# Performance work log

Measured on AMD Instinct MI355X. Metric: run time of the kernel, lower is better.

Reference implementation:

```python
import jax, jax.numpy as jnp
import numpy as np
import math

N, E, D, H = 1536, 49152, 512, 8
DH = D // H  # head dim = 64
SCALE = 256.0 * math.sqrt(2.0)  # rel_dists scaling in forward


def sinusoidal_pe(x, d):
    """x: [...] float positions -> [..., d] interleaved sin/cos encoding."""
    div = jnp.exp(jnp.arange(0, d, 2, dtype=jnp.float32) * (-math.log(10000.0) / d))
    ang = x[..., None] * div  # [..., d//2]
    return jnp.stack([jnp.sin(ang), jnp.cos(ang)], axis=-1).reshape(*x.shape, d)


def setup_inputs() -> dict:
    key = jax.random.key(0)
    ks = jax.random.split(key, 8)
    features = jax.random.normal(ks[0], (N, D), dtype=jnp.float32)
    edge_index = jax.random.randint(ks[1], (2, E), 0, N, dtype=jnp.int64)
    edge_attr = jax.random.uniform(ks[2], (E,), dtype=jnp.float32)  # normalized distances
    pos = jax.random.uniform(ks[3], (N, 2), dtype=jnp.float32)  # unused by forward
    s = 1.0 / math.sqrt(D)  # ~xavier-uniform bound sqrt(6/(D+D))... use simple symmetric init
    Wq = jax.random.uniform(ks[4], (D, D), minval=-s, maxval=s, dtype=jnp.float32)
    Wk = jax.random.uniform(ks[5], (D, D), minval=-s, maxval=s, dtype=jnp.float32)
    Wv = jax.random.uniform(ks[6], (D, D), minval=-s, maxval=s, dtype=jnp.float32)
    bq = jnp.zeros((D,), jnp.float32)
    bk = jnp.zeros((D,), jnp.float32)
    bv = jnp.zeros((D,), jnp.float32)
    return dict(features=features, edge_index=edge_index, edge_attr=edge_attr, pos=pos,
                Wq=Wq, bq=bq, Wk=Wk, bk=bk, Wv=Wv, bv=bv)


def reference(features, edge_index, edge_attr, pos, Wq, bq, Wk, bk, Wv, bv):
    # batch dim is 1 in the original (features.unsqueeze(0)); we omit it.
    q = (features @ Wq.T + bq).reshape(N, H, DH).transpose(1, 0, 2)  # [H,N,DH]
    k = (features @ Wk.T + bk).reshape(N, H, DH).transpose(1, 0, 2)
    v = (features @ Wv.T + bv).reshape(N, H, DH).transpose(1, 0, 2)

    qk = jnp.einsum('hqd,hrd->hqr', q, k)  # [H,N,N]

    # to_dense_adj: scatter-add edge_attr into dense [N,N], then scale
    rel = jnp.zeros((N, N), jnp.float32).at[edge_index[0], edge_index[1]].add(edge_attr) * SCALE
    # embed_k and embed_q are identical parameter-free sinusoidal encodings of rel
    rk = sinusoidal_pe(rel, DH)  # [N,N,DH]

    # original: qk + q.rk + k.rq + (q_repeat*k_repeat == qk)  => 2*qk + q.rk + k.rk
    logits = 2.0 * qk \
        + jnp.einsum('hqd,qrd->hqr', q, rk) \
        + jnp.einsum('hrd,qrd->hqr', k, rk)
    attn = jax.nn.softmax(logits / math.sqrt(DH), axis=-1)  # [H,N,N]

    out = jnp.einsum('hqr,hrd->hqd', attn, v)  # [H,N,DH]
    out = out.transpose(1, 0, 2).reshape(N, D)  # [N,D]
    return out.max(axis=0)  # [D] max-pool over nodes (MIL pooling)
```

## Files before the change

kernel.cpp:

```cpp
#include <hip/hip_runtime.h>
#include <cmath>


constexpr int Nn  = 1536;
constexpr int Dd  = 512;
constexpr int Hh  = 8;
constexpr int DHd = 64;
constexpr int SPLITS = 4;
constexpr float SCALE_F = 362.03867196751236f;
constexpr float M0 = 8.0f;

typedef float f4 __attribute__((ext_vector_type(4)));
typedef int   i4 __attribute__((ext_vector_type(4)));
typedef unsigned short us4 __attribute__((ext_vector_type(4)));
typedef __attribute__((ext_vector_type(4))) float f32x4;
typedef __attribute__((ext_vector_type(8))) short bf16x8;

__device__ inline unsigned short bf16_rne(float x) {
    unsigned u = __float_as_uint(x);
    unsigned r = u + 0x7fff + ((u >> 16) & 1);
    return (unsigned short)(r >> 16);
}
__device__ inline float bf16_tof(unsigned short h) {
    return __uint_as_float(((unsigned)h) << 16);
}
__device__ inline unsigned f2ord(float x) {
    unsigned b = __float_as_uint(x);
    return (b & 0x80000000u) ? ~b : (b | 0x80000000u);
}

__global__ __launch_bounds__(256) void setup_k(
    const float* __restrict__ feat,
    const float* __restrict__ Wq, const float* __restrict__ Wk, const float* __restrict__ Wv,
    unsigned short* __restrict__ pFh, unsigned short* __restrict__ pFl,
    unsigned short* __restrict__ pWh, unsigned short* __restrict__ pWl,
    float* __restrict__ rel, unsigned short* __restrict__ eid16,
    float* __restrict__ Obuf, float* __restrict__ Lbuf,
    float* __restrict__ qkodd, unsigned* __restrict__ ordmax)
{
    const int b = blockIdx.x, tid = threadIdx.x;
    if (b < 768) {
        int type = (b >= 384);
        int tg = (type ? (b - 384) : b) * 256 + tid;
        int L = tg & 63;
        int kc = (tg >> 6) & 15;
        int t10 = tg >> 10;
        const float* src;
        unsigned short *oh, *ol;
        int row, col;
        if (type == 0) {
            src = feat; oh = pFh; ol = pFl;
            row = t10 * 16 + (L & 15);
            col = kc * 32 + (L >> 4) * 8;
        } else {
            int z = t10 >> 5, nt = t10 & 31;
            src = (z == 0) ? Wq : (z == 1) ? Wk : Wv;
            oh = pWh; ol = pWl;
            row = nt * 16 + (L & 15);
            col = kc * 32 + (L >> 4) * 8;
        }
        f4 a = *(const f4*)(src + (size_t)row * Dd + col);
        f4 bb = *(const f4*)(src + (size_t)row * Dd + col + 4);
        float x[8];
        #pragma unroll
        for (int j = 0; j < 4; ++j) { x[j] = a[j]; x[4 + j] = bb[j]; }
        unsigned short hs[8], ls[8];
        #pragma unroll
        for (int j = 0; j < 8; ++j) {
            hs[j] = bf16_rne(x[j]);
            ls[j] = bf16_rne(x[j] - bf16_tof(hs[j]));
        }
        *(bf16x8*)(oh + (size_t)tg * 8) = *(bf16x8*)hs;
        *(bf16x8*)(ol + (size_t)tg * 8) = *(bf16x8*)ls;
    } else if (b < 3072) {
        size_t idx = (size_t)(b - 768) * 256 + tid;
        *(f4*)(rel + idx * 4) = (f4){0.f, 0.f, 0.f, 0.f};
        *(us4*)(eid16 + idx * 4) = (us4){0xFFFFu, 0xFFFFu, 0xFFFFu, 0xFFFFu};
    } else if (b < 3840) {
        size_t idx = (size_t)(b - 3072) * 256 + tid;
        *(f4*)(Obuf + idx * 4) = (f4){0.f, 0.f, 0.f, 0.f};
    } else if (b < 3852) {
        size_t idx = (size_t)(b - 3840) * 256 + tid;
        *(f4*)(Lbuf + idx * 4) = (f4){0.f, 0.f, 0.f, 0.f};
    } else if (b < 3876) {
        size_t idx = (size_t)(b - 3852) * 256 + tid;
        *(f4*)(qkodd + idx * 4) = (f4){0.f, 0.f, 0.f, 0.f};
    } else {
        int idx = (b - 3876) * 256 + tid;
        ordmax[idx] = 0x007FFFFFu;
    }
}

__global__ __launch_bounds__(256) void qkvm_k(
    const unsigned short* __restrict__ pFh, const unsigned short* __restrict__ pFl,
    const unsigned short* __restrict__ pWh, const unsigned short* __restrict__ pWl,
    const float* __restrict__ bq, const float* __restrict__ bk, const float* __restrict__ bv,
    float* __restrict__ Qo, float* __restrict__ Ko,
    float* __restrict__ qodd, float* __restrict__ kodd,
    unsigned short* __restrict__ pQh, unsigned short* __restrict__ pQl,
    unsigned short* __restrict__ pKh, unsigned short* __restrict__ pKl,
    unsigned short* __restrict__ pVh, unsigned short* __restrict__ pVl)
{
    const int z = blockIdx.z;
    const float* __restrict__ bias = (z == 0) ? bq : (z == 1) ? bk : bv;
    const int tid = threadIdx.x;
    const int L = tid & 63, wv = tid >> 6;
    const int l15 = L & 15, quad = L >> 4;
    const int mt0 = blockIdx.y * 4 + (wv & 1) * 2;
    const int nt0 = blockIdx.x * 4 + (wv >> 1) * 2;
    __shared__ float lds[4][32][33];

    f32x4 acc[2][2];
    #pragma unroll
    for (int i = 0; i < 2; ++i)
        #pragma unroll
        for (int j = 0; j < 2; ++j) acc[i][j] = (f32x4){0.f, 0.f, 0.f, 0.f};

    bf16x8 AH[2][2], AL[2][2], BH[2][2], BL[2][2];
    auto loadset = [&](int buf, int kc) {
        #pragma unroll
        for (int i = 0; i < 2; ++i) {
            size_t ao = ((size_t)((mt0 + i) * 16 + kc)) * 512 + L * 8;
            AH[buf][i] = *(const bf16x8*)(pFh + ao);
            AL[buf][i] = *(const bf16x8*)(pFl + ao);
            size_t bo = ((size_t)((z * 32 + nt0 + i) * 16 + kc)) * 512 + L * 8;
            BH[buf][i] = *(const bf16x8*)(pWh + bo);
            BL[buf][i] = *(const bf16x8*)(pWl + bo);
        }
    };
    auto mfmaset = [&](int buf) {
        #pragma unroll
        for (int i = 0; i < 2; ++i)
            #pragma unroll
            for (int j = 0; j < 2; ++j) {
                f32x4 a = acc[i][j];
                a = __builtin_amdgcn_mfma_f32_16x16x32_bf16(AH[buf][i], BH[buf][j], a, 0, 0, 0);
                a = __builtin_amdgcn_mfma_f32_16x16x32_bf16(AH[buf][i], BL[buf][j], a, 0, 0, 0);
                a = __builtin_amdgcn_mfma_f32_16x16x32_bf16(AL[buf][i], BH[buf][j], a, 0, 0, 0);
                a = __builtin_amdgcn_mfma_f32_16x16x32_bf16(AL[buf][i], BL[buf][j], a, 0, 0, 0);
                acc[i][j] = a;
            }
    };

    loadset(0, 0);
    #pragma unroll
    for (int kc = 0; kc < 16; kc += 2) {
        loadset(1, kc + 1);
        mfmaset(0);
        if (kc + 2 < 16) loadset(0, kc + 2);
        mfmaset(1);
    }

    float o_[2][2][4];
    #pragma unroll
    for (int i = 0; i < 2; ++i)
        #pragma unroll
        for (int j = 0; j < 2; ++j) {
            float b = bias[(nt0 + j) * 16 + l15];
            #pragma unroll
            for (int reg = 0; reg < 4; ++reg) o_[i][j][reg] = acc[i][j][reg] + b;
        }
    if (z < 2) {
        float* __restrict__ outp = (z == 0) ? Qo : Ko;
        #pragma unroll
        for (int i = 0; i < 2; ++i) {
            int row0 = (mt0 + i) * 16 + quad * 4;
            #pragma unroll
            for (int j = 0; j < 2; ++j) {
                int col = (nt0 + j) * 16 + l15;
                #pragma unroll
                for (int reg = 0; reg < 4; ++reg)
                    outp[(size_t)(row0 + reg) * Dd + col] = o_[i][j][reg];
            }
        }
        float* __restrict__ odst = (z == 0) ? qodd : kodd;
        const int h = blockIdx.x;
        #pragma unroll
        for (int i = 0; i < 2; ++i) {
            #pragma unroll
            for (int reg = 0; reg < 4; ++reg) {
                float v = (l15 & 1) ? (o_[i][0][reg] + o_[i][1][reg]) : 0.f;
                #pragma unroll
                for (int o = 1; o < 16; o <<= 1) v += __shfl_xor(v, o);
                if (l15 == 0) {
                    int row = (mt0 + i) * 16 + quad * 4 + reg;
                    atomicAdd(&odst[row * Hh + h], v);
                }
            }
        }
    }
    #pragma unroll
    for (int i = 0; i < 2; ++i)
        #pragma unroll
        for (int j = 0; j < 2; ++j)
            #pragma unroll
            for (int reg = 0; reg < 4; ++reg)
                lds[wv][i * 16 + quad * 4 + reg][j * 16 + l15] = o_[i][j][reg];

    const int h = blockIdx.x;
    if (z < 2) {
        unsigned short* __restrict__ oh = z ? pKh : pQh;
        unsigned short* __restrict__ ol = z ? pKl : pQl;
        const int kc = wv >> 1;
        const float sc = z ? 1.0f : 0.25f;
        #pragma unroll
        for (int i = 0; i < 2; ++i) {
            float x[8]; unsigned short hs[8], ls[8];
            #pragma unroll
            for (int j2 = 0; j2 < 8; ++j2)
                x[j2] = lds[wv][i * 16 + l15][quad * 8 + j2] * sc;
            #pragma unroll
            for (int j2 = 0; j2 < 8; ++j2) {
                hs[j2] = bf16_rne(x[j2]);
                ls[j2] = bf16_rne(x[j2] - bf16_tof(hs[j2]));
            }
            size_t off = ((size_t)((h * 96 + mt0 + i) * 2 + kc)) * 512 + L * 8;
            *(bf16x8*)(oh + off) = *(bf16x8*)hs;
            *(bf16x8*)(ol + off) = *(bf16x8*)ls;
        }
    } else {
        const int rc = blockIdx.y * 2 + (wv & 1);
        #pragma unroll
        for (int dtl = 0; dtl < 2; ++dtl) {
            int dt = (wv >> 1) * 2 + dtl;
            float x[8]; unsigned short hs[8], ls[8];
            #pragma unroll
            for (int j2 = 0; j2 < 8; ++j2)
                x[j2] = lds[wv][quad * 8 + j2][dtl * 16 + l15];
            #pragma unroll
            for (int j2 = 0; j2 < 8; ++j2) {
                hs[j2] = bf16_rne(x[j2]);
                ls[j2] = bf16_rne(x[j2] - bf16_tof(hs[j2]));
            }
            size_t off = ((size_t)((h * 48 + rc) * 4 + dt)) * 512 + L * 8;
            *(bf16x8*)(pVh + off) = *(bf16x8*)hs;
            *(bf16x8*)(pVl + off) = *(bf16x8*)ls;
        }
    }
}

__global__ __launch_bounds__(256) void scatter_k(
    const int* __restrict__ raw, const float* __restrict__ attr,
    float* __restrict__ rel, unsigned short* __restrict__ eid16,
    int* __restrict__ idxn, int E)
{
    int e = blockIdx.x * 256 + threadIdx.x;
    if (e >= E) return;
    int acc = 0;
    #pragma unroll
    for (int i = 0; i < 16; ++i) acc |= raw[2 * i + 1];
    int s, t;
    if (acc == 0) { s = raw[2 * e]; t = raw[2 * (E + e)]; }
    else          { s = raw[e];     t = raw[E + e]; }
    idxn[e] = s; idxn[E + e] = t;
    size_t off = (size_t)s * Nn + t;
    atomicAdd(rel + off, attr[e] * SCALE_F);
    eid16[off] = (unsigned short)e;
}

__global__ __launch_bounds__(256) void delta_k(
    const int* __restrict__ idxn, const float* __restrict__ rel,
    const float* __restrict__ Q, const float* __restrict__ K,
    const float* __restrict__ qodd, const float* __restrict__ kodd,
    float* __restrict__ delta8, int E)
{
    int t = blockIdx.x * 256 + threadIdx.x;
    if (t >= E * Hh) return;
    int e = t >> 3, h = t & 7;
    int qi = idxn[e], ri = idxn[E + e];
    float x = rel[(size_t)qi * Nn + ri];
    const float* qrow = Q + (size_t)qi * Dd + h * DHd;
    const float* krow = K + (size_t)ri * Dd + h * DHd;
    float acc = 0.f;
    #pragma unroll
    for (int i = 0; i < 32; i += 2) {
        float dd0 = 0.15915494309189535f * __builtin_amdgcn_exp2f(-0.4152410118609203f * (float)i);
        float dd1 = 0.15915494309189535f * __builtin_amdgcn_exp2f(-0.4152410118609203f * (float)(i + 1));
        float r0 = x * dd0; r0 -= floorf(r0);
        float r1 = x * dd1; r1 -= floorf(r1);
        float s0 = __builtin_amdgcn_sinf(r0), c0 = __builtin_amdgcn_cosf(r0);
        float s1 = __builtin_amdgcn_sinf(r1), c1 = __builtin_amdgcn_cosf(r1);
        f4 q4 = *(const f4*)(qrow + 2 * i);
        f4 k4 = *(const f4*)(krow + 2 * i);
        acc += (q4[0] + k4[0]) * s0 + (q4[1] + k4[1]) * c0
             + (q4[2] + k4[2]) * s1 + (q4[3] + k4[3]) * c1;
    }
    delta8[(size_t)e * Hh + h] = 0.125f * (acc - qodd[qi * Hh + h] - kodd[ri * Hh + h]);
}

__global__ __launch_bounds__(64, 3) void flash7_k(
    const unsigned short* __restrict__ pQh, const unsigned short* __restrict__ pQl,
    const unsigned short* __restrict__ pKh, const unsigned short* __restrict__ pKl,
    const unsigned short* __restrict__ pVh, const unsigned short* __restrict__ pVl,
    const unsigned short* __restrict__ eid16, const float* __restrict__ delta8,
    const float* __restrict__ kodd,
    float* __restrict__ Obuf, float* __restrict__ Lbuf)
{
    const int qt = blockIdx.x, h = blockIdx.y, s = blockIdx.z;
    const int L = threadIdx.x, quad = L >> 4, l15 = L & 15;
    const int q0 = qt * 16;
    __shared__ unsigned short phi[16][80];
    __shared__ unsigned short plo[16][80];

    bf16x8 qh[2], ql[2];
    #pragma unroll
    for (int kc = 0; kc < 2; ++kc) {
        size_t off = ((size_t)((h * 96 + qt) * 2 + kc)) * 512 + L * 8;
        qh[kc] = *(const bf16x8*)(pQh + off);
        ql[kc] = *(const bf16x8*)(pQl + off);
    }

    f32x4 O[4];
    float lsum[4];
    #pragma unroll
    for (int r = 0; r < 4; ++r) { lsum[r] = 0.f; O[r] = (f32x4){0.f, 0.f, 0.f, 0.f}; }

    const int NT = 24 / SPLITS;
    const int Tbase = s * NT;

    bf16x8 kh0[4], kh1[4], kl0[4], kl1[4];
    {
        const int r0 = Tbase * 64;
        #pragma unroll
        for (int nt = 0; nt < 4; ++nt) {
            size_t b0 = ((size_t)((h * 96 + (r0 >> 4) + nt) * 2)) * 512 + L * 8;
            kh0[nt] = *(const bf16x8*)(pKh + b0);
            kh1[nt] = *(const bf16x8*)(pKh + b0 + 512);
            kl0[nt] = *(const bf16x8*)(pKl + b0);
            kl1[nt] = *(const bf16x8*)(pKl + b0 + 512);
        }
    }

    float kvcur[4], dcur[16];
    {
        const int r0 = Tbase * 64;
        int ecur[16];
        #pragma unroll
        for (int nt = 0; nt < 4; ++nt) {
            kvcur[nt] = 0.125f * kodd[(size_t)(r0 + nt * 16 + l15) * Hh + h];
            #pragma unroll
            for (int reg = 0; reg < 4; ++reg) {
                unsigned short uv = eid16[(size_t)(q0 + quad * 4 + reg) * Nn + r0 + nt * 16 + l15];
                ecur[nt * 4 + reg] = (uv == 0xFFFFu) ? -1 : (int)uv;
            }
        }
        #pragma unroll
        for (int i = 0; i < 16; ++i) {
            int e = ecur[i];
            float d = delta8[(size_t)(e < 0 ? 0 : e) * Hh + h];
            dcur[i] = (e >= 0) ? d : 0.f;
        }
    }

    for (int T = 0; T < NT; ++T) {
        const int r0 = (Tbase + T) * 64;
        const bool more = (T + 1 < NT);

        int   enxt[16];
        float kvnxt[4];
        if (more) {
            const int r1 = r0 + 64;
            #pragma unroll
            for (int nt = 0; nt < 4; ++nt) {
                kvnxt[nt] = 0.125f * kodd[(size_t)(r1 + nt * 16 + l15) * Hh + h];
                #pragma unroll
                for (int reg = 0; reg < 4; ++reg) {
                    unsigned short uv = eid16[(size_t)(q0 + quad * 4 + reg) * Nn + r1 + nt * 16 + l15];
                    enxt[nt * 4 + reg] = (uv == 0xFFFFu) ? -1 : (int)uv;
                }
            }
        }

        bf16x8 vh0[4], vh1[4], vl0[4], vl1[4];
        #pragma unroll
        for (int dt = 0; dt < 4; ++dt) {
            size_t vb = ((size_t)((h * 48 + (r0 >> 5)) * 4 + dt)) * 512 + L * 8;
            vh0[dt] = *(const bf16x8*)(pVh + vb);
            vh1[dt] = *(const bf16x8*)(pVh + vb + 2048);
            vl0[dt] = *(const bf16x8*)(pVl + vb);
            vl1[dt] = *(const bf16x8*)(pVl + vb + 2048);
        }

        f32x4 S[4];
        #pragma unroll
        for (int nt = 0; nt < 4; ++nt) {
            f32x4 a = {0.f, 0.f, 0.f, 0.f};
            a = __builtin_amdgcn_mfma_f32_16x16x32_bf16(qh[0], kh0[nt], a, 0, 0, 0);
            a = __builtin_amdgcn_mfma_f32_16x16x32_bf16(qh[1], kh1[nt], a, 0, 0, 0);
            a = __builtin_amdgcn_mfma_f32_16x16x32_bf16(qh[0], kl0[nt], a, 0, 0, 0);
            a = __builtin_amdgcn_mfma_f32_16x16x32_bf16(qh[1], kl1[nt], a, 0, 0, 0);
            a = __builtin_amdgcn_mfma_f32_16x16x32_bf16(ql[0], kh0[nt], a, 0, 0, 0);
            a = __builtin_amdgcn_mfma_f32_16x16x32_bf16(ql[1], kh1[nt], a, 0, 0, 0);
            S[nt] = a;
        }

        if (more) {
            const int r1 = r0 + 64;
            #pragma unroll
            for (int nt = 0; nt < 4; ++nt) {
                size_t b0 = ((size_t)((h * 96 + (r1 >> 4) + nt) * 2)) * 512 + L * 8;
                kh0[nt] = *(const bf16x8*)(pKh + b0);
                kh1[nt] = *(const bf16x8*)(pKh + b0 + 512);
                kl0[nt] = *(const bf16x8*)(pKl + b0);
                kl1[nt] = *(const bf16x8*)(pKl + b0 + 512);
            }
        }

        #pragma unroll
        for (int reg = 0; reg < 4; ++reg) {
            float p[4];
            #pragma unroll
            for (int nt = 0; nt < 4; ++nt) {
                p[nt] = __expf(S[nt][reg] + kvcur[nt] + dcur[nt * 4 + reg] - M0);
                lsum[reg] += p[nt];
                unsigned short hi = bf16_rne(p[nt]);
                phi[quad * 4 + reg][nt * 16 + l15] = hi;
                plo[quad * 4 + reg][nt * 16 + l15] = bf16_rne(p[nt] - bf16_tof(hi));
            }
        }

        bf16x8 ph[2], pl[2];
        #pragma unroll
        for (int kc2 = 0; kc2 < 2; ++kc2) {
            ph[kc2] = *(const bf16x8*)&phi[l15][kc2 * 32 + quad * 8];
            pl[kc2] = *(const bf16x8*)&plo[l15][kc2 * 32 + quad * 8];
        }

        #pragma unroll
        for (int dt = 0; dt < 4; ++dt) {
            f32x4 a = O[dt];
            a = __builtin_amdgcn_mfma_f32_16x16x32_bf16(ph[0], vh0[dt], a, 0, 0, 0);
            a = __builtin_amdgcn_mfma_f32_16x16x32_bf16(ph[1], vh1[dt], a, 0, 0, 0);
            a = __builtin_amdgcn_mfma_f32_16x16x32_bf16(ph[0], vl0[dt], a, 0, 0, 0);
            a = __builtin_amdgcn_mfma_f32_16x16x32_bf16(ph[1], vl1[dt], a, 0, 0, 0);
            a = __builtin_amdgcn_mfma_f32_16x16x32_bf16(pl[0], vh0[dt], a, 0, 0, 0);
            a = __builtin_amdgcn_mfma_f32_16x16x32_bf16(pl[1], vh1[dt], a, 0, 0, 0);
            O[dt] = a;
        }

        if (more) {
            #pragma unroll
            for (int i = 0; i < 16; ++i) {
                int e = enxt[i];
                float d = delta8[(size_t)(e < 0 ? 0 : e) * Hh + h];
                dcur[i] = (e >= 0) ? d : 0.f;
            }
            #pragma unroll
            for (int nt = 0; nt < 4; ++nt) kvcur[nt] = kvnxt[nt];
        }
    }

    #pragma unroll
    for (int reg = 0; reg < 4; ++reg) {
        #pragma unroll
        for (int o = 1; o < 16; o <<= 1) lsum[reg] += __shfl_xor(lsum[reg], o);
    }

    #pragma unroll
    for (int dt = 0; dt < 4; ++dt)
        #pragma unroll
        for (int reg = 0; reg < 4; ++reg)
            atomicAdd(&Obuf[(size_t)(q0 + quad * 4 + reg) * Dd + h * DHd + dt * 16 + l15],
                      O[dt][reg]);
    if (l15 == 0) {
        #pragma unroll
        for (int reg = 0; reg < 4; ++reg)
            atomicAdd(&Lbuf[(size_t)h * Nn + q0 + quad * 4 + reg], lsum[reg]);
    }
}

__global__ __launch_bounds__(256) void finalize_mp_k(
    const float* __restrict__ Obuf, const float* __restrict__ Lbuf,
    unsigned* __restrict__ ordmax)
{
    const int b = blockIdx.x;
    const int t = threadIdx.x;
    const int cg = (t & 127) * 4;
    const int h = cg >> 6;
    const int rh = t >> 7;
    f4 mx = {-3.0e38f, -3.0e38f, -3.0e38f, -3.0e38f};
    for (int r = 0; r < 8; ++r) {
        int q = b * 16 + rh * 8 + r;
        float inv = 1.0f / Lbuf[(size_t)h * Nn + q];
        f4 ov = *(const f4*)(Obuf + (size_t)q * Dd + cg);
        #pragma unroll
        for (int c = 0; c < 4; ++c) mx[c] = fmaxf(mx[c], ov[c] * inv);
    }
    #pragma unroll
    for (int c = 0; c < 4; ++c) atomicMax(&ordmax[cg + c], f2ord(mx[c]));
}

__global__ void decode_k(const unsigned* __restrict__ ordmax, float* __restrict__ outp)
{
    int t = blockIdx.x * 256 + threadIdx.x;
    if (t >= Dd) return;
    unsigned u = ordmax[t];
    outp[t] = (u & 0x80000000u) ? __uint_as_float(u ^ 0x80000000u) : __uint_as_float(~u);
}

extern "C" void kernel_launch(void* const* d_in, const int* in_sizes, int n_in,
                              void* d_out, int out_size, void* d_ws, size_t ws_size,
                              hipStream_t stream)
{
    const float* feat   = (const float*)d_in[0];
    const int*   rawidx = (const int*)d_in[1];
    const float* attr   = (const float*)d_in[2];
    const float* Wq = (const float*)d_in[4];
    const float* bq = (const float*)d_in[5];
    const float* Wk = (const float*)d_in[6];
    const float* bk = (const float*)d_in[7];
    const float* Wv = (const float*)d_in[8];
    const float* bv = (const float*)d_in[9];
    float* outp = (float*)d_out;
    const int E = in_sizes[2];

    const size_t ND_ = (size_t)Nn * Dd;
    const size_t NN_ = (size_t)Nn * Nn;
    const size_t PK_ = (size_t)Hh * 96 * 2 * 512;
    float* ws    = (float*)d_ws;
    float* Q     = ws;
    float* K     = Q + ND_;
    unsigned short* pFh = (unsigned short*)(K + ND_);
    unsigned short* pFl = pFh + PK_;
    unsigned short* pWh = pFl + PK_;
    unsigned short* pWl = pWh + PK_;
    float* rel   = (float*)(pWl + PK_);
    unsigned short* eid16 = (unsigned short*)(rel + NN_);
    float* delta8 = (float*)(eid16 + NN_);
    float* qodd  = delta8 + (size_t)E * Hh;
    float* kodd  = qodd + (size_t)Nn * Hh;
    int*   idxn  = (int*)(kodd + (size_t)Nn * Hh);
    unsigned short* pQh = (unsigned short*)(idxn + 2 * E);
    unsigned short* pQl = pQh + PK_;
    unsigned short* pKh = pQl + PK_;
    unsigned short* pKl = pKh + PK_;
    unsigned short* pVh = pKl + PK_;
    unsigned short* pVl = pVh + PK_;
    float* Obuf  = (float*)(pVl + PK_);
    float* Lbuf  = Obuf + ND_;
    unsigned* ordmax = (unsigned*)(Lbuf + (size_t)Hh * Nn);

    setup_k<<<3878, 256, 0, stream>>>(feat, Wq, Wk, Wv, pFh, pFl, pWh, pWl,
                                      rel, eid16, Obuf, Lbuf, qodd, ordmax);
    qkvm_k<<<dim3(8, 24, 3), 256, 0, stream>>>(pFh, pFl, pWh, pWl, bq, bk, bv,
                                               Q, K, qodd, kodd,
                                               pQh, pQl, pKh, pKl, pVh, pVl);
    scatter_k<<<(E + 255) / 256, 256, 0, stream>>>(rawidx, attr, rel, eid16, idxn, E);
    delta_k<<<(E * Hh + 255) / 256, 256, 0, stream>>>(idxn, rel, Q, K, qodd, kodd, delta8, E);
    flash7_k<<<dim3(96, 8, SPLITS), 64, 0, stream>>>(pQh, pQl, pKh, pKl, pVh, pVl,
                                                     eid16, delta8, kodd, Obuf, Lbuf);
    finalize_mp_k<<<96, 256, 0, stream>>>(Obuf, Lbuf, ordmax);
    decode_k<<<(Dd + 255) / 256, 256, 0, stream>>>(ordmax, outp);
}
```

Baseline: 201.6 us.

## Cut setup memsets, drop fp32 Q/K, write split partials instead of atomics

```diff
diff --git a/kernel.cpp b/kernel.cpp
--- a/kernel.cpp
+++ b/kernel.cpp
@@ -32,11 +32,12 @@
 __global__ __launch_bounds__(256) void setup_k(
     const float* __restrict__ feat,
     const float* __restrict__ Wq, const float* __restrict__ Wk, const float* __restrict__ Wv,
+    const int* __restrict__ raw,
     unsigned short* __restrict__ pFh, unsigned short* __restrict__ pFl,
     unsigned short* __restrict__ pWh, unsigned short* __restrict__ pWl,
-    float* __restrict__ rel, unsigned short* __restrict__ eid16,
-    float* __restrict__ Obuf, float* __restrict__ Lbuf,
-    float* __restrict__ qkodd, unsigned* __restrict__ ordmax)
+    unsigned short* __restrict__ eid16, float* __restrict__ rel,
+    int* __restrict__ idxn, float* __restrict__ qkodd,
+    unsigned* __restrict__ ordmax, int E)
 {
     const int b = blockIdx.x, tid = threadIdx.x;
     if (b < 768) {
@@ -74,20 +75,25 @@
         *(bf16x8*)(ol + (size_t)tg * 8) = *(bf16x8*)ls;
     } else if (b < 3072) {
         size_t idx = (size_t)(b - 768) * 256 + tid;
-        *(f4*)(rel + idx * 4) = (f4){0.f, 0.f, 0.f, 0.f};
         *(us4*)(eid16 + idx * 4) = (us4){0xFFFFu, 0xFFFFu, 0xFFFFu, 0xFFFFu};
-    } else if (b < 3840) {
+    } else if (b < 3096) {
         size_t idx = (size_t)(b - 3072) * 256 + tid;
-        *(f4*)(Obuf + idx * 4) = (f4){0.f, 0.f, 0.f, 0.f};
-    } else if (b < 3852) {
-        size_t idx = (size_t)(b - 3840) * 256 + tid;
-        *(f4*)(Lbuf + idx * 4) = (f4){0.f, 0.f, 0.f, 0.f};
-    } else if (b < 3876) {
-        size_t idx = (size_t)(b - 3852) * 256 + tid;
         *(f4*)(qkodd + idx * 4) = (f4){0.f, 0.f, 0.f, 0.f};
+    } else if (b < 3098) {
+        int idx = (b - 3096) * 256 + tid;
+        ordmax[idx] = 0x007FFFFFu;
     } else {
-        int idx = (b - 3876) * 256 + tid;
-        ordmax[idx] = 0x007FFFFFu;
+        int e = (b - 3098) * 256 + tid;
+        if (e < E) {
+            int acc = 0;
+            #pragma unroll
+            for (int i = 0; i < 16; ++i) acc |= raw[2 * i + 1];
+            int s, t;
+            if (acc == 0) { s = raw[2 * e]; t = raw[2 * (E + e)]; }
+            else          { s = raw[e];     t = raw[E + e]; }
+            idxn[e] = s; idxn[E + e] = t;
+            rel[(size_t)s * Nn + t] = 0.f;
+        }
     }
 }
 
@@ -95,7 +101,6 @@
     const unsigned short* __restrict__ pFh, const unsigned short* __restrict__ pFl,
     const unsigned short* __restrict__ pWh, const unsigned short* __restrict__ pWl,
     const float* __restrict__ bq, const float* __restrict__ bk, const float* __restrict__ bv,
-    float* __restrict__ Qo, float* __restrict__ Ko,
     float* __restrict__ qodd, float* __restrict__ kodd,
     unsigned short* __restrict__ pQh, unsigned short* __restrict__ pQl,
     unsigned short* __restrict__ pKh, unsigned short* __restrict__ pKl,
@@ -160,21 +165,9 @@
             #pragma unroll
             for (int reg = 0; reg < 4; ++reg) o_[i][j][reg] = acc[i][j][reg] + b;
         }
+    const int h = blockIdx.x;
     if (z < 2) {
-        float* __restrict__ outp = (z == 0) ? Qo : Ko;
-        #pragma unroll
-        for (int i = 0; i < 2; ++i) {
-            int row0 = (mt0 + i) * 16 + quad * 4;
-            #pragma unroll
-            for (int j = 0; j < 2; ++j) {
-                int col = (nt0 + j) * 16 + l15;
-                #pragma unroll
-                for (int reg = 0; reg < 4; ++reg)
-                    outp[(size_t)(row0 + reg) * Dd + col] = o_[i][j][reg];
-            }
-        }
         float* __restrict__ odst = (z == 0) ? qodd : kodd;
-        const int h = blockIdx.x;
         #pragma unroll
         for (int i = 0; i < 2; ++i) {
             #pragma unroll
@@ -197,7 +190,6 @@
             for (int reg = 0; reg < 4; ++reg)
                 lds[wv][i * 16 + quad * 4 + reg][j * 16 + l15] = o_[i][j][reg];
 
-    const int h = blockIdx.x;
     if (z < 2) {
         unsigned short* __restrict__ oh = z ? pKh : pQh;
         unsigned short* __restrict__ ol = z ? pKl : pQl;
@@ -240,19 +232,12 @@
 }
 
 __global__ __launch_bounds__(256) void scatter_k(
-    const int* __restrict__ raw, const float* __restrict__ attr,
-    float* __restrict__ rel, unsigned short* __restrict__ eid16,
-    int* __restrict__ idxn, int E)
+    const int* __restrict__ idxn, const float* __restrict__ attr,
+    float* __restrict__ rel, unsigned short* __restrict__ eid16, int E)
 {
     int e = blockIdx.x * 256 + threadIdx.x;
     if (e >= E) return;
-    int acc = 0;
-    #pragma unroll
-    for (int i = 0; i < 16; ++i) acc |= raw[2 * i + 1];
-    int s, t;
-    if (acc == 0) { s = raw[2 * e]; t = raw[2 * (E + e)]; }
-    else          { s = raw[e];     t = raw[E + e]; }
-    idxn[e] = s; idxn[E + e] = t;
+    int s = idxn[e], t = idxn[E + e];
     size_t off = (size_t)s * Nn + t;
     atomicAdd(rel + off, attr[e] * SCALE_F);
     eid16[off] = (unsigned short)e;
@@ -260,7 +245,8 @@
 
 __global__ __launch_bounds__(256) void delta_k(
     const int* __restrict__ idxn, const float* __restrict__ rel,
-    const float* __restrict__ Q, const float* __restrict__ K,
+    const unsigned short* __restrict__ pQh, const unsigned short* __restrict__ pQl,
+    const unsigned short* __restrict__ pKh, const unsigned short* __restrict__ pKl,
     const float* __restrict__ qodd, const float* __restrict__ kodd,
     float* __restrict__ delta8, int E)
 {
@@ -269,34 +255,50 @@
     int e = t >> 3, h = t & 7;
     int qi = idxn[e], ri = idxn[E + e];
     float x = rel[(size_t)qi * Nn + ri];
-    const float* qrow = Q + (size_t)qi * Dd + h * DHd;
-    const float* krow = K + (size_t)ri * Dd + h * DHd;
     float acc = 0.f;
     #pragma unroll
-    for (int i = 0; i < 32; i += 2) {
-        float dd0 = 0.15915494309189535f * __builtin_amdgcn_exp2f(-0.4152410118609203f * (float)i);
-        float dd1 = 0.15915494309189535f * __builtin_amdgcn_exp2f(-0.4152410118609203f * (float)(i + 1));
-        float r0 = x * dd0; r0 -= floorf(r0);
-        float r1 = x * dd1; r1 -= floorf(r1);
-        float s0 = __builtin_amdgcn_sinf(r0), c0 = __builtin_amdgcn_cosf(r0);
-        float s1 = __builtin_amdgcn_sinf(r1), c1 = __builtin_amdgcn_cosf(r1);
-        f4 q4 = *(const f4*)(qrow + 2 * i);
-        f4 k4 = *(const f4*)(krow + 2 * i);
-        acc += (q4[0] + k4[0]) * s0 + (q4[1] + k4[1]) * c0
-             + (q4[2] + k4[2]) * s1 + (q4[3] + k4[3]) * c1;
+    for (int kc = 0; kc < 2; ++kc) {
+        #pragma unroll
+        for (int qd = 0; qd < 4; ++qd) {
+            size_t qoff = ((size_t)((h * 96 + (qi >> 4)) * 2 + kc)) * 512
+                        + (size_t)(qd * 16 + (qi & 15)) * 8;
+            size_t koff = ((size_t)((h * 96 + (ri >> 4)) * 2 + kc)) * 512
+                        + (size_t)(qd * 16 + (ri & 15)) * 8;
+            bf16x8 qh8 = *(const bf16x8*)(pQh + qoff);
+            bf16x8 ql8 = *(const bf16x8*)(pQl + qoff);
+            bf16x8 kh8 = *(const bf16x8*)(pKh + koff);
+            bf16x8 kl8 = *(const bf16x8*)(pKl + koff);
+            const int ib = kc * 16 + qd * 4;
+            #pragma unroll
+            for (int jp = 0; jp < 4; ++jp) {
+                float dd = 0.15915494309189535f
+                         * __builtin_amdgcn_exp2f(-0.4152410118609203f * (float)(ib + jp));
+                float r = x * dd; r -= floorf(r);
+                float sv = __builtin_amdgcn_sinf(r), cv = __builtin_amdgcn_cosf(r);
+                float qe = 4.f * (bf16_tof((unsigned short)qh8[2 * jp]) +
+                                  bf16_tof((unsigned short)ql8[2 * jp]))
+                         + bf16_tof((unsigned short)kh8[2 * jp])
+                         + bf16_tof((unsigned short)kl8[2 * jp]);
+                float qo = 4.f * (bf16_tof((unsigned short)qh8[2 * jp + 1]) +
+                                  bf16_tof((unsigned short)ql8[2 * jp + 1]))
+                         + bf16_tof((unsigned short)kh8[2 * jp + 1])
+                         + bf16_tof((unsigned short)kl8[2 * jp + 1]);
+                acc += qe * sv + qo * cv;
+            }
+        }
     }
     delta8[(size_t)e * Hh + h] = 0.125f * (acc - qodd[qi * Hh + h] - kodd[ri * Hh + h]);
 }
 
-__global__ __launch_bounds__(64, 3) void flash7_k(
+__global__ __launch_bounds__(64, 3) void flash8_k(
     const unsigned short* __restrict__ pQh, const unsigned short* __restrict__ pQl,
     const unsigned short* __restrict__ pKh, const unsigned short* __restrict__ pKl,
     const unsigned short* __restrict__ pVh, const unsigned short* __restrict__ pVl,
     const unsigned short* __restrict__ eid16, const float* __restrict__ delta8,
     const float* __restrict__ kodd,
-    float* __restrict__ Obuf, float* __restrict__ Lbuf)
-{
-    const int qt = blockIdx.x, h = blockIdx.y, s = blockIdx.z;
+    float* __restrict__ Opart, float* __restrict__ Lpart)
+{
+    const int s = blockIdx.x, qt = blockIdx.y, h = blockIdx.z;
     const int L = threadIdx.x, quad = L >> 4, l15 = L & 15;
     const int q0 = qt * 16;
     __shared__ unsigned short phi[16][80];
@@ -460,31 +462,38 @@
     for (int dt = 0; dt < 4; ++dt)
         #pragma unroll
         for (int reg = 0; reg < 4; ++reg)
-            atomicAdd(&Obuf[(size_t)(q0 + quad * 4 + reg) * Dd + h * DHd + dt * 16 + l15],
-                      O[dt][reg]);
+            Opart[((size_t)(s * Hh + h) * Nn + q0 + quad * 4 + reg) * 64 + dt * 16 + l15] = O[dt][reg];
     if (l15 == 0) {
         #pragma unroll
         for (int reg = 0; reg < 4; ++reg)
-            atomicAdd(&Lbuf[(size_t)h * Nn + q0 + quad * 4 + reg], lsum[reg]);
-    }
-}
-
-__global__ __launch_bounds__(256) void finalize_mp_k(
-    const float* __restrict__ Obuf, const float* __restrict__ Lbuf,
+            Lpart[(size_t)(s * Hh + h) * Nn + q0 + quad * 4 + reg] = lsum[reg];
+    }
+}
+
+__global__ __launch_bounds__(256) void combine_mp_k(
+    const float* __restrict__ Opart, const float* __restrict__ Lpart,
     unsigned* __restrict__ ordmax)
 {
     const int b = blockIdx.x;
     const int t = threadIdx.x;
     const int cg = (t & 127) * 4;
-    const int h = cg >> 6;
+    const int h = cg >> 6, d = cg & 63;
     const int rh = t >> 7;
     f4 mx = {-3.0e38f, -3.0e38f, -3.0e38f, -3.0e38f};
     for (int r = 0; r < 8; ++r) {
         int q = b * 16 + rh * 8 + r;
-        float inv = 1.0f / Lbuf[(size_t)h * Nn + q];
-        f4 ov = *(const f4*)(Obuf + (size_t)q * Dd + cg);
-        #pragma unroll
-        for (int c = 0; c < 4; ++c) mx[c] = fmaxf(mx[c], ov[c] * inv);
+        float l = 0.f;
+        f4 o = {0.f, 0.f, 0.f, 0.f};
+        #pragma unroll
+        for (int s2 = 0; s2 < SPLITS; ++s2) {
+            l += Lpart[(size_t)(s2 * Hh + h) * Nn + q];
+            f4 ov = *(const f4*)(Opart + ((size_t)(s2 * Hh + h) * Nn + q) * 64 + d);
+            #pragma unroll
+            for (int c = 0; c < 4; ++c) o[c] += ov[c];
+        }
+        float inv = 1.0f / l;
+        #pragma unroll
+        for (int c = 0; c < 4; ++c) mx[c] = fmaxf(mx[c], o[c] * inv);
     }
     #pragma unroll
     for (int c = 0; c < 4; ++c) atomicMax(&ordmax[cg + c], f2ord(mx[c]));
@@ -513,18 +522,16 @@
     const float* bv = (const float*)d_in[9];
     float* outp = (float*)d_out;
     const int E = in_sizes[2];
-
-    const size_t ND_ = (size_t)Nn * Dd;
+    const int EB = (E + 255) / 256;
+
     const size_t NN_ = (size_t)Nn * Nn;
     const size_t PK_ = (size_t)Hh * 96 * 2 * 512;
-    float* ws    = (float*)d_ws;
-    float* Q     = ws;
-    float* K     = Q + ND_;
-    unsigned short* pFh = (unsigned short*)(K + ND_);
+    float* ws = (float*)d_ws;
+    unsigned short* pFh = (unsigned short*)ws;
     unsigned short* pFl = pFh + PK_;
     unsigned short* pWh = pFl + PK_;
     unsigned short* pWl = pWh + PK_;
-    float* rel   = (float*)(pWl + PK_);
+    float* rel = (float*)(pWl + PK_);
     unsigned short* eid16 = (unsigned short*)(rel + NN_);
     float* delta8 = (float*)(eid16 + NN_);
     float* qodd  = delta8 + (size_t)E * Hh;
@@ -536,19 +543,21 @@
     unsigned short* pKl = pKh + PK_;
     unsigned short* pVh = pKl + PK_;
     unsigned short* pVl = pVh + PK_;
-    float* Obuf  = (float*)(pVl + PK_);
-    float* Lbuf  = Obuf + ND_;
-    unsigned* ordmax = (unsigned*)(Lbuf + (size_t)Hh * Nn);
-
-    setup_k<<<3878, 256, 0, stream>>>(feat, Wq, Wk, Wv, pFh, pFl, pWh, pWl,
-                                      rel, eid16, Obuf, Lbuf, qodd, ordmax);
+    float* Lpart = (float*)(pVl + PK_);
+    unsigned* ordmax = (unsigned*)(Lpart + (size_t)SPLITS * Hh * Nn);
+    float* Opart = ws;
+
+    setup_k<<<3098 + EB, 256, 0, stream>>>(feat, Wq, Wk, Wv, rawidx,
+                                           pFh, pFl, pWh, pWl,
+                                           eid16, rel, idxn, qodd, ordmax, E);
     qkvm_k<<<dim3(8, 24, 3), 256, 0, stream>>>(pFh, pFl, pWh, pWl, bq, bk, bv,
-                                               Q, K, qodd, kodd,
+                                               qodd, kodd,
                                                pQh, pQl, pKh, pKl, pVh, pVl);
-    scatter_k<<<(E + 255) / 256, 256, 0, stream>>>(rawidx, attr, rel, eid16, idxn, E);
-    delta_k<<<(E * Hh + 255) / 256, 256, 0, stream>>>(idxn, rel, Q, K, qodd, kodd, delta8, E);
-    flash7_k<<<dim3(96, 8, SPLITS), 64, 0, stream>>>(pQh, pQl, pKh, pKl, pVh, pVl,
-                                                     eid16, delta8, kodd, Obuf, Lbuf);
-    finalize_mp_k<<<96, 256, 0, stream>>>(Obuf, Lbuf, ordmax);
+    scatter_k<<<EB, 256, 0, stream>>>(idxn, attr, rel, eid16, E);
+    delta_k<<<(E * Hh + 255) / 256, 256, 0, stream>>>(idxn, rel, pQh, pQl, pKh, pKl,
+                                                      qodd, kodd, delta8, E);
+    flash8_k<<<dim3(SPLITS, 96, 8), 64, 0, stream>>>(pQh, pQl, pKh, pKl, pVh, pVl,
+                                                     eid16, delta8, kodd, Opart, Lpart);
+    combine_mp_k<<<96, 256, 0, stream>>>(Opart, Lpart, ordmax);
     decode_k<<<(Dd + 255) / 256, 256, 0, stream>>>(ordmax, outp);
 }
```

After: 223.9 us. +11.0%, slower.
